# Performance work log

Measured on AMD Instinct MI355X. Metric: run time of the kernel, lower is better.

Reference implementation:

```python
import jax, jax.numpy as jnp
import numpy as np
import math

H = 16  # num heads
NEG = -1e9


def setup_inputs() -> dict:
    key = jax.random.key(0)
    ks = jax.random.split(key, 12)
    B, S, D = 2, 2048, 1024
    inp = {
        "query": jax.random.normal(ks[0], (B, S, D), jnp.float32),
        "key": jax.random.normal(ks[1], (B, S, D), jnp.float32),
        "value": jax.random.normal(ks[2], (B, S, D), jnp.float32),
        "mask": jax.random.randint(ks[3], (B, 1, S), 0, 2, jnp.int32),
        "wq": jax.random.normal(ks[4], (D, D), jnp.float32) * 0.02,
        "bq": jnp.zeros((D,), jnp.float32),
        "wk": jax.random.normal(ks[5], (D, D), jnp.float32) * 0.02,
        "bk": jnp.zeros((D,), jnp.float32),
        "wv": jax.random.normal(ks[6], (D, D), jnp.float32) * 0.02,
        "bv": jnp.zeros((D,), jnp.float32),
        "wo": jax.random.normal(ks[7], (D, D), jnp.float32) * 0.02,
        "bo": jnp.zeros((D,), jnp.float32),
    }
    return inp


def reference(query, key, value, mask, wq, bq, wk, bk, wv, bv, wo, bo):
    B, S, D = query.shape
    dk = D // H

    def proj(x, w, b):
        # torch Linear: x @ w.T + b ; then split heads -> [B, H, S, dk]
        y = x @ w.T + b
        return y.reshape(B, -1, H, dk).transpose(0, 2, 1, 3)

    q = proj(query, wq, bq)
    k = proj(key, wk, bk)
    v = proj(value, wv, bv)

    scores = jnp.einsum("bhqd,bhkd->bhqk", q, k) / math.sqrt(dk)  # [B,H,S,S]

    m = mask[:, None, :, :]  # [B,1,1,S] (mask.unsqueeze(1) in torch)
    scores = jnp.where(m == 0, NEG, scores)            # key-side padding mask
    scores = jnp.where(jnp.swapaxes(m, -2, -1) == 0, NEG, scores)  # query-side mask (q_len>1)

    p_attn = jax.nn.softmax(scores, axis=-1)
    # dropout p=0 / eval mode -> identity
    ctx = jnp.einsum("bhqk,bhkd->bhqd", p_attn, v)  # [B,H,S,dk]
    ctx = ctx.transpose(0, 2, 1, 3).reshape(B, S, H * dk)
    out = ctx @ wo.T + bo
    return out
```

## Files before the change

### kernel.cpp

```cpp
#include <hip/hip_runtime.h>
#include <hip/hip_bf16.h>

#define SEQ 2048
#define DIM 1024
#define NH  16
#define DK  64
#define NA  (2 * SEQ * DIM)
#define NW  (DIM * DIM)
#define PSTR 72
#define ESTR 136
#define FSTR 132
#define QSCALE 0.18033688011112042f

typedef __attribute__((ext_vector_type(4))) float f32x4;
typedef __attribute__((ext_vector_type(8))) __bf16 bf16x8;
typedef __attribute__((ext_vector_type(4))) __bf16 bf16x4;

__device__ __forceinline__ f32x4 mfma16(bf16x8 a, bf16x8 b, f32x4 c) {
  return __builtin_amdgcn_mfma_f32_16x16x32_bf16(a, b, c, 0, 0, 0);
}
__device__ __forceinline__ void async_load16(const void* g, void* l) {
  __builtin_amdgcn_global_load_lds(
      (const __attribute__((address_space(1))) void*)g,
      (__attribute__((address_space(3))) void*)l, 16, 0, 0);
}
__device__ __forceinline__ int swz(int row, int chunk) {
  return row * 8 + (chunk ^ (row & 7));
}

__global__ __launch_bounds__(256) void cvt_kernel(
    const float* __restrict__ s0, const float* __restrict__ s1,
    const float* __restrict__ s2, const float* __restrict__ s3,
    const float* __restrict__ s4, const float* __restrict__ s5,
    const float* __restrict__ s6,
    __hip_bfloat16* __restrict__ d0, __hip_bfloat16* __restrict__ d1,
    __hip_bfloat16* __restrict__ d2, __hip_bfloat16* __restrict__ d3,
    __hip_bfloat16* __restrict__ d4, __hip_bfloat16* __restrict__ d5,
    __hip_bfloat16* __restrict__ d6) {
  const int id = blockIdx.x;
  const float* s;
  __hip_bfloat16* d;
  int bid;
  if (id < 6144) {
    int t = id >> 11;
    bid = id & 2047;
    s = (t == 0) ? s0 : ((t == 1) ? s1 : s2);
    d = (t == 0) ? d0 : ((t == 1) ? d1 : d2);
  } else {
    int t = (id - 6144) >> 9;
    bid = (id - 6144) & 511;
    s = (t == 0) ? s3 : ((t == 1) ? s4 : ((t == 2) ? s5 : s6));
    d = (t == 0) ? d3 : ((t == 1) ? d4 : ((t == 2) ? d5 : d6));
  }
  size_t i = ((size_t)bid * 256 + threadIdx.x) * 8;
  float4 a = *(const float4*)(s + i);
  float4 b = *(const float4*)(s + i + 4);
  bf16x8 v = {(__bf16)a.x, (__bf16)a.y, (__bf16)a.z, (__bf16)a.w,
              (__bf16)b.x, (__bf16)b.y, (__bf16)b.z, (__bf16)b.w};
  *(bf16x8*)(d + i) = v;
}

__device__ __forceinline__ void gemm_stage(
    const __hip_bfloat16* __restrict__ X, const __hip_bfloat16* __restrict__ W,
    __hip_bfloat16* A, __hip_bfloat16* B, int m0, int n0, int k0,
    int w, int lane) {
  for (int r = 0; r < 4; ++r) {
    int cbase = r * 256 + w * 64;
    int c = cbase + lane, row = c >> 3, cs = c & 7;
    int off = cs ^ (row & 7);
    async_load16((const char*)(X + (size_t)(m0 + row) * DIM + k0) + off * 16,
                 (char*)A + cbase * 16);
    async_load16((const char*)(W + (size_t)(n0 + row) * DIM + k0) + off * 16,
                 (char*)B + cbase * 16);
  }
}

__device__ __forceinline__ void gemm_mainloop(
    const __hip_bfloat16* __restrict__ X, const __hip_bfloat16* __restrict__ W,
    __hip_bfloat16* lds, int m0, int n0, f32x4 acc[4][4]) {
  const int tid = threadIdx.x, lane = tid & 63, w = tid >> 6;
  const int quad = lane >> 4, l15 = lane & 15;
  const int wm = (w >> 1) * 64, wn = (w & 1) * 64;

  f32x4 z = {0.f, 0.f, 0.f, 0.f};
  for (int mi = 0; mi < 4; ++mi)
    for (int ni = 0; ni < 4; ++ni) acc[mi][ni] = z;

  gemm_stage(X, W, lds, lds + 8192, m0, n0, 0, w, lane);
  __syncthreads();

  for (int it = 0; it < 16; ++it) {
    __hip_bfloat16* Ac = lds + (it & 1) * 16384;
    __hip_bfloat16* Bc = Ac + 8192;
    if (it < 15) {
      __hip_bfloat16* An = lds + ((it + 1) & 1) * 16384;
      gemm_stage(X, W, An, An + 8192, m0, n0, (it + 1) * 64, w, lane);
    }
    for (int kk = 0; kk < 2; ++kk) {
      bf16x8 a[4], b[4];
      for (int mi = 0; mi < 4; ++mi)
        a[mi] = *(const bf16x8*)(Ac + swz(wm + mi * 16 + l15, kk * 4 + quad) * 8);
      for (int ni = 0; ni < 4; ++ni)
        b[ni] = *(const bf16x8*)(Bc + swz(wn + ni * 16 + l15, kk * 4 + quad) * 8);
      for (int mi = 0; mi < 4; ++mi)
        for (int ni = 0; ni < 4; ++ni)
          acc[mi][ni] = mfma16(a[mi], b[ni], acc[mi][ni]);
    }
    __syncthreads();
  }
}

__global__ __launch_bounds__(256) void qkv_proj_kernel(
    const __hip_bfloat16* __restrict__ xq, const __hip_bfloat16* __restrict__ xk,
    const __hip_bfloat16* __restrict__ xv,
    const __hip_bfloat16* __restrict__ wq, const __hip_bfloat16* __restrict__ wk,
    const __hip_bfloat16* __restrict__ wv,
    const float* __restrict__ bq, const float* __restrict__ bk,
    const float* __restrict__ bv,
    __hip_bfloat16* __restrict__ q_ws, __hip_bfloat16* __restrict__ k_ws,
    __hip_bfloat16* __restrict__ vt_ws) {
  __shared__ __align__(16) __hip_bfloat16 S_lds[4 * 8192];

  const int z = blockIdx.z;
  const __hip_bfloat16* X = (z == 0) ? xq : ((z == 1) ? xk : xv);
  const __hip_bfloat16* W = (z == 0) ? wq : ((z == 1) ? wk : wv);
  const float* bias = (z == 0) ? bq : ((z == 1) ? bk : bv);
  const float f = (z == 0) ? QSCALE : 1.0f;

  const int m0 = blockIdx.y * 128, n0 = blockIdx.x * 128;
  f32x4 acc[4][4];
  gemm_mainloop(X, W, S_lds, m0, n0, acc);

  const int tid = threadIdx.x, lane = tid & 63, w = tid >> 6;
  const int quad = lane >> 4, l15 = lane & 15;
  const int wm = (w >> 1) * 64, wn = (w & 1) * 64;

  if (z != 2) {
    __hip_bfloat16* out = (z == 0) ? q_ws : k_ws;
    for (int mi = 0; mi < 4; ++mi)
      for (int ni = 0; ni < 4; ++ni) {
        const float bv_ = bias[n0 + wn + ni * 16 + l15];
        for (int r = 0; r < 4; ++r)
          S_lds[(wm + mi * 16 + quad * 4 + r) * ESTR + wn + ni * 16 + l15] =
              __float2bfloat16((acc[mi][ni][r] + bv_) * f);
      }
    __syncthreads();
    for (int r2 = 0; r2 < 8; ++r2) {
      int c = r2 * 256 + tid;
      int row = c >> 4, j = c & 15;
      int m = m0 + row, b = m >> 11, s = m & 2047;
      int n = n0 + j * 8, h = n >> 6, d = n & 63;
      *(uint4*)(out + ((size_t)(b * NH + h) * SEQ + s) * DK + d) =
          *(const uint4*)(S_lds + row * ESTR + j * 8);
    }
  } else {
    for (int mi = 0; mi < 4; ++mi)
      for (int ni = 0; ni < 4; ++ni) {
        const int n_local = wn + ni * 16 + l15;
        const float bv_ = bias[n0 + n_local];
        bf16x4 tv;
        for (int r = 0; r < 4; ++r) tv[r] = (__bf16)(acc[mi][ni][r] + bv_);
        *(bf16x4*)(S_lds + n_local * ESTR + wm + mi * 16 + quad * 4) = tv;
      }
    __syncthreads();
    const int b = m0 >> 11, s_base = m0 & 2047;
    for (int r2 = 0; r2 < 8; ++r2) {
      int c2 = r2 * 256 + tid;
      int nrow = c2 >> 4, moff = (c2 & 15) * 8;
      int n = n0 + nrow, h = n >> 6, d = n & 63;
      *(uint4*)(vt_ws + ((size_t)(b * NH + h) * DK + d) * SEQ + s_base + moff) =
          *(const uint4*)(S_lds + nrow * ESTR + moff);
    }
  }
}

__global__ __launch_bounds__(512) void attn_kernel(
    const __hip_bfloat16* __restrict__ qg, const __hip_bfloat16* __restrict__ kg,
    const __hip_bfloat16* __restrict__ vtg, const int* __restrict__ mask,
    __hip_bfloat16* __restrict__ ctx) {
  __shared__ __align__(16) __hip_bfloat16 QP_lds[128 * PSTR];
  __shared__ __align__(16) __hip_bfloat16 K_lds[2][64 * 64];
  __shared__ __align__(16) __hip_bfloat16 V_lds[2][64 * 64];
  __shared__ float bias_lds[SEQ];

  const int tid = threadIdx.x, lane = tid & 63, w = tid >> 6;
  const int quad = lane >> 4, l15 = lane & 15;
  const int bh = blockIdx.y, b = bh >> 4, h = bh & 15;
  const int q0 = blockIdx.x * 128;
  const size_t head = (size_t)bh * SEQ * DK;
  const size_t vthead = (size_t)bh * DK * SEQ;

  for (int i = tid; i < SEQ; i += 512)
    bias_lds[i] = mask[b * SEQ + i] ? 0.f : -1e9f;

  for (int r = 0; r < 2; ++r) {
    int cbase = r * 512 + w * 64;
    int c = cbase + lane, row = c >> 3, cs = c & 7;
    int off = cs ^ (row & 7);
    async_load16((const char*)(qg + head + (size_t)(q0 + row) * DK) + off * 16,
                 (char*)QP_lds + cbase * 16);
  }
  {
    int row = tid >> 3, cs = tid & 7;
    int off = cs ^ (row & 7);
    async_load16((const char*)(kg + head + (size_t)row * DK) + off * 16,
                 (char*)K_lds[0] + tid * 16);
    async_load16((const char*)(vtg + vthead + (size_t)row * SEQ) + off * 16,
                 (char*)V_lds[0] + tid * 16);
  }
  __syncthreads();

  bf16x8 qf[2];
  for (int kk = 0; kk < 2; ++kk)
    qf[kk] = *(const bf16x8*)(QP_lds + swz(w * 16 + l15, kk * 4 + quad) * 8);
  const int qmv = mask[b * SEQ + q0 + w * 16 + l15];

  __hip_bfloat16* P_lds = QP_lds;
  const bf16x8 ones = {(__bf16)1.f, (__bf16)1.f, (__bf16)1.f, (__bf16)1.f,
                       (__bf16)1.f, (__bf16)1.f, (__bf16)1.f, (__bf16)1.f};

  f32x4 z = {0.f, 0.f, 0.f, 0.f};
  f32x4 o_acc[4];
  for (int di = 0; di < 4; ++di) o_acc[di] = z;
  f32x4 o_sum = z;

  for (int t = 0; t < 32; ++t) {
    const int cur = t & 1;
    if (t < 31) {
      const int k1 = (t + 1) * 64;
      int row = tid >> 3, cs = tid & 7;
      int off = cs ^ (row & 7);
      async_load16((const char*)(kg + head + (size_t)(k1 + row) * DK) + off * 16,
                   (char*)K_lds[1 - cur] + tid * 16);
      async_load16((const char*)(vtg + vthead + (size_t)row * SEQ + k1) + off * 16,
                   (char*)V_lds[1 - cur] + tid * 16);
    }
    const int k0 = t * 64;

    f32x4 s_acc[4];
    for (int mi = 0; mi < 4; ++mi)
      s_acc[mi] = *(const f32x4*)(bias_lds + k0 + mi * 16 + quad * 4);
    for (int kk = 0; kk < 2; ++kk) {
      bf16x8 ak[4];
      for (int mi = 0; mi < 4; ++mi)
        ak[mi] = *(const bf16x8*)(K_lds[cur] + swz(mi * 16 + l15, kk * 4 + quad) * 8);
      for (int mi = 0; mi < 4; ++mi)
        s_acc[mi] = mfma16(ak[mi], qf[kk], s_acc[mi]);
    }

    for (int mi = 0; mi < 4; ++mi) {
      bf16x4 pk;
      for (int r = 0; r < 4; ++r) {
        float s2 = qmv ? s_acc[mi][r] : 0.f;
        pk[r] = (__bf16)__builtin_amdgcn_exp2f(s2);
      }
      *(bf16x4*)(P_lds + (w * 16 + l15) * PSTR + mi * 16 + quad * 4) = pk;
    }

    for (int kk = 0; kk < 2; ++kk) {
      bf16x8 bp = *(const bf16x8*)(P_lds + (w * 16 + l15) * PSTR + kk * 32 + quad * 8);
      bf16x8 av[4];
      for (int di = 0; di < 4; ++di)
        av[di] = *(const bf16x8*)(V_lds[cur] + swz(di * 16 + l15, kk * 4 + quad) * 8);
      for (int di = 0; di < 4; ++di)
        o_acc[di] = mfma16(av[di], bp, o_acc[di]);
      o_sum = mfma16(ones, bp, o_sum);
    }
    __syncthreads();
  }

  const float inv = 1.f / o_sum[0];

  for (int di = 0; di < 4; ++di) {
    bf16x4 ov;
    for (int r = 0; r < 4; ++r) ov[r] = (__bf16)(o_acc[di][r] * inv);
    *(bf16x4*)(P_lds + (w * 16 + l15) * PSTR + di * 16 + quad * 4) = ov;
  }
  __syncthreads();
  for (int r = 0; r < 2; ++r) {
    int c = r * 512 + tid, row = c >> 3, off = c & 7;
    *(uint4*)(ctx + (size_t)(b * SEQ + q0 + row) * DIM + h * DK + off * 8) =
        *(const uint4*)(P_lds + row * PSTR + off * 8);
  }
}

__global__ __launch_bounds__(256) void out_proj_kernel(
    const __hip_bfloat16* __restrict__ ctx, const __hip_bfloat16* __restrict__ wo,
    const float* __restrict__ bo, float* __restrict__ out) {
  __shared__ __align__(16) char S_raw[128 * FSTR * 4];
  __hip_bfloat16* S_lds = (__hip_bfloat16*)S_raw;

  const int m0 = blockIdx.y * 128, n0 = blockIdx.x * 128;
  f32x4 acc[4][4];
  gemm_mainloop(ctx, wo, S_lds, m0, n0, acc);

  const int tid = threadIdx.x, lane = tid & 63, w = tid >> 6;
  const int quad = lane >> 4, l15 = lane & 15;
  const int wm = (w >> 1) * 64, wn = (w & 1) * 64;
  float* epi = (float*)S_raw;

  for (int mi = 0; mi < 4; ++mi)
    for (int ni = 0; ni < 4; ++ni) {
      const float bv_ = bo[n0 + wn + ni * 16 + l15];
      for (int r = 0; r < 4; ++r)
        epi[(wm + mi * 16 + quad * 4 + r) * FSTR + wn + ni * 16 + l15] =
            acc[mi][ni][r] + bv_;
    }
  __syncthreads();
  for (int r2 = 0; r2 < 16; ++r2) {
    int c = r2 * 256 + tid;
    int row = c >> 5, j = c & 31;
    *(float4*)(out + (size_t)(m0 + row) * DIM + n0 + j * 4) =
        *(const float4*)(epi + row * FSTR + j * 4);
  }
}

extern "C" void kernel_launch(void* const* d_in, const int* in_sizes, int n_in,
                              void* d_out, int out_size, void* d_ws, size_t ws_size,
                              hipStream_t stream) {
  const float* query = (const float*)d_in[0];
  const float* key   = (const float*)d_in[1];
  const float* value = (const float*)d_in[2];
  const int*   mask  = (const int*)d_in[3];
  const float* wq = (const float*)d_in[4];
  const float* bq = (const float*)d_in[5];
  const float* wk = (const float*)d_in[6];
  const float* bk = (const float*)d_in[7];
  const float* wv = (const float*)d_in[8];
  const float* bv = (const float*)d_in[9];
  const float* wo = (const float*)d_in[10];
  const float* bo = (const float*)d_in[11];
  float* out = (float*)d_out;

  char* ws = (char*)d_ws;
  const size_t SZA = (size_t)NA * 2;
  const size_t SZW = (size_t)NW * 2;
  __hip_bfloat16* xq  = (__hip_bfloat16*)(ws);
  __hip_bfloat16* xk  = (__hip_bfloat16*)(ws + SZA);
  __hip_bfloat16* xv  = (__hip_bfloat16*)(ws + 2 * SZA);
  __hip_bfloat16* wqb = (__hip_bfloat16*)(ws + 3 * SZA);
  __hip_bfloat16* wkb = (__hip_bfloat16*)(ws + 3 * SZA + SZW);
  __hip_bfloat16* wvb = (__hip_bfloat16*)(ws + 3 * SZA + 2 * SZW);
  __hip_bfloat16* wob = (__hip_bfloat16*)(ws + 3 * SZA + 3 * SZW);
  __hip_bfloat16* q_ws  = (__hip_bfloat16*)(ws + 3 * SZA + 4 * SZW);
  __hip_bfloat16* k_ws  = (__hip_bfloat16*)(ws + 4 * SZA + 4 * SZW);
  __hip_bfloat16* vt_ws = (__hip_bfloat16*)(ws + 5 * SZA + 4 * SZW);
  __hip_bfloat16* ctx_ws = xq;

  cvt_kernel<<<dim3(8192), dim3(256), 0, stream>>>(
      query, key, value, wq, wk, wv, wo, xq, xk, xv, wqb, wkb, wvb, wob);
  qkv_proj_kernel<<<dim3(8, 32, 3), dim3(256), 0, stream>>>(
      xq, xk, xv, wqb, wkb, wvb, bq, bk, bv, q_ws, k_ws, vt_ws);
  attn_kernel<<<dim3(16, 32), dim3(512), 0, stream>>>(q_ws, k_ws, vt_ws, mask, ctx_ws);
  out_proj_kernel<<<dim3(8, 32), dim3(256), 0, stream>>>(ctx_ws, wob, bo, out);
}
```

Measured before the change: 225.9 us.

## Give each attention wave two 16-row query tiles, halving block size

Cuts the attention block from 8 waves to 4, with each wave now covering 32 query rows (two 16-row MFMA tiles) instead of 16. Each K and V fragment read from LDS is reused across two query tiles, which halves LDS reads of K/V per MFMA. In exchange, per-wave register use grows (doubled score and output accumulators), fewer waves per block can hide latency, and each thread issues twice as many async loads.

```diff
diff --git a/kernel.cpp b/kernel.cpp
--- a/kernel.cpp
+++ b/kernel.cpp
@@ -174,7 +174,7 @@
   }
 }
 
-__global__ __launch_bounds__(512) void attn_kernel(
+__global__ __launch_bounds__(256) void attn_kernel(
     const __hip_bfloat16* __restrict__ qg, const __hip_bfloat16* __restrict__ kg,
     const __hip_bfloat16* __restrict__ vtg, const int* __restrict__ mask,
     __hip_bfloat16* __restrict__ ctx) {
@@ -190,95 +190,111 @@
   const size_t head = (size_t)bh * SEQ * DK;
   const size_t vthead = (size_t)bh * DK * SEQ;
 
-  for (int i = tid; i < SEQ; i += 512)
+  for (int i = tid; i < SEQ; i += 256)
     bias_lds[i] = mask[b * SEQ + i] ? 0.f : -1e9f;
 
-  for (int r = 0; r < 2; ++r) {
-    int cbase = r * 512 + w * 64;
+  for (int r = 0; r < 4; ++r) {
+    int cbase = r * 256 + w * 64;
     int c = cbase + lane, row = c >> 3, cs = c & 7;
     int off = cs ^ (row & 7);
     async_load16((const char*)(qg + head + (size_t)(q0 + row) * DK) + off * 16,
                  (char*)QP_lds + cbase * 16);
   }
-  {
-    int row = tid >> 3, cs = tid & 7;
+  for (int r = 0; r < 2; ++r) {
+    int cbase = r * 256 + w * 64;
+    int c = cbase + lane, row = c >> 3, cs = c & 7;
     int off = cs ^ (row & 7);
     async_load16((const char*)(kg + head + (size_t)row * DK) + off * 16,
-                 (char*)K_lds[0] + tid * 16);
+                 (char*)K_lds[0] + cbase * 16);
     async_load16((const char*)(vtg + vthead + (size_t)row * SEQ) + off * 16,
-                 (char*)V_lds[0] + tid * 16);
+                 (char*)V_lds[0] + cbase * 16);
   }
   __syncthreads();
 
-  bf16x8 qf[2];
+  bf16x8 qf[2][2];
   for (int kk = 0; kk < 2; ++kk)
-    qf[kk] = *(const bf16x8*)(QP_lds + swz(w * 16 + l15, kk * 4 + quad) * 8);
-  const int qmv = mask[b * SEQ + q0 + w * 16 + l15];
+    for (int ni = 0; ni < 2; ++ni)
+      qf[kk][ni] = *(const bf16x8*)(QP_lds + swz(w * 32 + ni * 16 + l15, kk * 4 + quad) * 8);
+  int qmv[2];
+  for (int ni = 0; ni < 2; ++ni)
+    qmv[ni] = mask[b * SEQ + q0 + w * 32 + ni * 16 + l15];
 
   __hip_bfloat16* P_lds = QP_lds;
   const bf16x8 ones = {(__bf16)1.f, (__bf16)1.f, (__bf16)1.f, (__bf16)1.f,
                        (__bf16)1.f, (__bf16)1.f, (__bf16)1.f, (__bf16)1.f};
 
   f32x4 z = {0.f, 0.f, 0.f, 0.f};
-  f32x4 o_acc[4];
-  for (int di = 0; di < 4; ++di) o_acc[di] = z;
-  f32x4 o_sum = z;
+  f32x4 o_acc[2][4];
+  for (int ni = 0; ni < 2; ++ni)
+    for (int di = 0; di < 4; ++di) o_acc[ni][di] = z;
+  f32x4 o_sum[2] = {z, z};
 
   for (int t = 0; t < 32; ++t) {
     const int cur = t & 1;
     if (t < 31) {
       const int k1 = (t + 1) * 64;
-      int row = tid >> 3, cs = tid & 7;
-      int off = cs ^ (row & 7);
-      async_load16((const char*)(kg + head + (size_t)(k1 + row) * DK) + off * 16,
-                   (char*)K_lds[1 - cur] + tid * 16);
-      async_load16((const char*)(vtg + vthead + (size_t)row * SEQ + k1) + off * 16,
-                   (char*)V_lds[1 - cur] + tid * 16);
+      for (int r = 0; r < 2; ++r) {
+        int cbase = r * 256 + w * 64;
+        int c = cbase + lane, row = c >> 3, cs = c & 7;
+        int off = cs ^ (row & 7);
+        async_load16((const char*)(kg + head + (size_t)(k1 + row) * DK) + off * 16,
+                     (char*)K_lds[1 - cur] + cbase * 16);
+        async_load16((const char*)(vtg + vthead + (size_t)row * SEQ + k1) + off * 16,
+                     (char*)V_lds[1 - cur] + cbase * 16);
+      }
     }
     const int k0 = t * 64;
 
-    f32x4 s_acc[4];
-    for (int mi = 0; mi < 4; ++mi)
-      s_acc[mi] = *(const f32x4*)(bias_lds + k0 + mi * 16 + quad * 4);
+    f32x4 s_acc[4][2];
+    for (int mi = 0; mi < 4; ++mi) {
+      f32x4 kb = *(const f32x4*)(bias_lds + k0 + mi * 16 + quad * 4);
+      for (int ni = 0; ni < 2; ++ni) s_acc[mi][ni] = kb;
+    }
     for (int kk = 0; kk < 2; ++kk) {
       bf16x8 ak[4];
       for (int mi = 0; mi < 4; ++mi)
         ak[mi] = *(const bf16x8*)(K_lds[cur] + swz(mi * 16 + l15, kk * 4 + quad) * 8);
       for (int mi = 0; mi < 4; ++mi)
-        s_acc[mi] = mfma16(ak[mi], qf[kk], s_acc[mi]);
-    }
-
-    for (int mi = 0; mi < 4; ++mi) {
-      bf16x4 pk;
-      for (int r = 0; r < 4; ++r) {
-        float s2 = qmv ? s_acc[mi][r] : 0.f;
-        pk[r] = (__bf16)__builtin_amdgcn_exp2f(s2);
-      }
-      *(bf16x4*)(P_lds + (w * 16 + l15) * PSTR + mi * 16 + quad * 4) = pk;
-    }
+        for (int ni = 0; ni < 2; ++ni)
+          s_acc[mi][ni] = mfma16(ak[mi], qf[kk][ni], s_acc[mi][ni]);
+    }
+
+    for (int mi = 0; mi < 4; ++mi)
+      for (int ni = 0; ni < 2; ++ni) {
+        bf16x4 pk;
+        for (int r = 0; r < 4; ++r) {
+          float s2 = qmv[ni] ? s_acc[mi][ni][r] : 0.f;
+          pk[r] = (__bf16)__builtin_amdgcn_exp2f(s2);
+        }
+        *(bf16x4*)(P_lds + (w * 32 + ni * 16 + l15) * PSTR + mi * 16 + quad * 4) = pk;
+      }
 
     for (int kk = 0; kk < 2; ++kk) {
-      bf16x8 bp = *(const bf16x8*)(P_lds + (w * 16 + l15) * PSTR + kk * 32 + quad * 8);
-      bf16x8 av[4];
+      bf16x8 av[4], bp[2];
       for (int di = 0; di < 4; ++di)
         av[di] = *(const bf16x8*)(V_lds[cur] + swz(di * 16 + l15, kk * 4 + quad) * 8);
-      for (int di = 0; di < 4; ++di)
-        o_acc[di] = mfma16(av[di], bp, o_acc[di]);
-      o_sum = mfma16(ones, bp, o_sum);
+      for (int ni = 0; ni < 2; ++ni)
+        bp[ni] = *(const bf16x8*)(P_lds + (w * 32 + ni * 16 + l15) * PSTR + kk * 32 + quad * 8);
+      for (int ni = 0; ni < 2; ++ni) {
+        for (int di = 0; di < 4; ++di)
+          o_acc[ni][di] = mfma16(av[di], bp[ni], o_acc[ni][di]);
+        o_sum[ni] = mfma16(ones, bp[ni], o_sum[ni]);
+      }
     }
     __syncthreads();
   }
 
-  const float inv = 1.f / o_sum[0];
-
-  for (int di = 0; di < 4; ++di) {
-    bf16x4 ov;
-    for (int r = 0; r < 4; ++r) ov[r] = (__bf16)(o_acc[di][r] * inv);
-    *(bf16x4*)(P_lds + (w * 16 + l15) * PSTR + di * 16 + quad * 4) = ov;
-  }
+  const float inv[2] = {1.f / o_sum[0][0], 1.f / o_sum[1][0]};
+
+  for (int ni = 0; ni < 2; ++ni)
+    for (int di = 0; di < 4; ++di) {
+      bf16x4 ov;
+      for (int r = 0; r < 4; ++r) ov[r] = (__bf16)(o_acc[ni][di][r] * inv[ni]);
+      *(bf16x4*)(P_lds + (w * 32 + ni * 16 + l15) * PSTR + di * 16 + quad * 4) = ov;
+    }
   __syncthreads();
-  for (int r = 0; r < 2; ++r) {
-    int c = r * 512 + tid, row = c >> 3, off = c & 7;
+  for (int r = 0; r < 4; ++r) {
+    int c = r * 256 + tid, row = c >> 3, off = c & 7;
     *(uint4*)(ctx + (size_t)(b * SEQ + q0 + row) * DIM + h * DK + off * 8) =
         *(const uint4*)(P_lds + row * PSTR + off * 8);
   }
@@ -351,6 +367,6 @@
       query, key, value, wq, wk, wv, wo, xq, xk, xv, wqb, wkb, wvb, wob);
   qkv_proj_kernel<<<dim3(8, 32, 3), dim3(256), 0, stream>>>(
       xq, xk, xv, wqb, wkb, wvb, bq, bk, bv, q_ws, k_ws, vt_ws);
-  attn_kernel<<<dim3(16, 32), dim3(512), 0, stream>>>(q_ws, k_ws, vt_ws, mask, ctx_ws);
+  attn_kernel<<<dim3(16, 32), dim3(256), 0, stream>>>(q_ws, k_ws, vt_ws, mask, ctx_ws);
   out_proj_kernel<<<dim3(8, 32), dim3(256), 0, stream>>>(ctx_ws, wob, bo, out);
 }
```

After: 243.4 us. +7.8%, slower.

## Store K/V in MFMA fragment order and load attention operands directly from global

Applied to the files above, without the earlier changes.

The QKV projection now writes K and V^T in a pre-swizzled, per-lane fragment layout, so the attention kernel can read MFMA operands straight from global or L2 into registers. This removes the K/V LDS double buffering, the async copies and the per-tile __syncthreads. The mask-to-bias conversion moves into one extra block of the convert kernel, and Q fragments are also read directly from global. The cost is that each of the 8 waves in a block now fetches the same K/V fragments from global separately instead of sharing one LDS copy, which relies on the cache hierarchy to absorb the repeated loads.

```diff
diff --git a/kernel.cpp b/kernel.cpp
--- a/kernel.cpp
+++ b/kernel.cpp
@@ -32,12 +32,17 @@
     const float* __restrict__ s0, const float* __restrict__ s1,
     const float* __restrict__ s2, const float* __restrict__ s3,
     const float* __restrict__ s4, const float* __restrict__ s5,
-    const float* __restrict__ s6,
+    const float* __restrict__ s6, const int* __restrict__ mask,
     __hip_bfloat16* __restrict__ d0, __hip_bfloat16* __restrict__ d1,
     __hip_bfloat16* __restrict__ d2, __hip_bfloat16* __restrict__ d3,
     __hip_bfloat16* __restrict__ d4, __hip_bfloat16* __restrict__ d5,
-    __hip_bfloat16* __restrict__ d6) {
+    __hip_bfloat16* __restrict__ d6, float* __restrict__ biasg) {
   const int id = blockIdx.x;
+  if (id == 8192) {
+    for (int i = threadIdx.x; i < 2 * SEQ; i += 256)
+      biasg[i] = mask[i] ? 0.f : -1e9f;
+    return;
+  }
   const float* s;
   __hip_bfloat16* d;
   int bid;
@@ -117,8 +122,8 @@
     const __hip_bfloat16* __restrict__ wv,
     const float* __restrict__ bq, const float* __restrict__ bk,
     const float* __restrict__ bv,
-    __hip_bfloat16* __restrict__ q_ws, __hip_bfloat16* __restrict__ k_ws,
-    __hip_bfloat16* __restrict__ vt_ws) {
+    __hip_bfloat16* __restrict__ q_ws, __hip_bfloat16* __restrict__ k_t,
+    __hip_bfloat16* __restrict__ vt_t) {
   __shared__ __align__(16) __hip_bfloat16 S_lds[4 * 8192];
 
   const int z = blockIdx.z;
@@ -134,9 +139,9 @@
   const int tid = threadIdx.x, lane = tid & 63, w = tid >> 6;
   const int quad = lane >> 4, l15 = lane & 15;
   const int wm = (w >> 1) * 64, wn = (w & 1) * 64;
+  const int b = m0 >> 11, tbase = (m0 & 2047) >> 6, hbase = n0 >> 6;
 
   if (z != 2) {
-    __hip_bfloat16* out = (z == 0) ? q_ws : k_ws;
     for (int mi = 0; mi < 4; ++mi)
       for (int ni = 0; ni < 4; ++ni) {
         const float bv_ = bias[n0 + wn + ni * 16 + l15];
@@ -145,13 +150,25 @@
               __float2bfloat16((acc[mi][ni][r] + bv_) * f);
       }
     __syncthreads();
-    for (int r2 = 0; r2 < 8; ++r2) {
-      int c = r2 * 256 + tid;
-      int row = c >> 4, j = c & 15;
-      int m = m0 + row, b = m >> 11, s = m & 2047;
-      int n = n0 + j * 8, h = n >> 6, d = n & 63;
-      *(uint4*)(out + ((size_t)(b * NH + h) * SEQ + s) * DK + d) =
-          *(const uint4*)(S_lds + row * ESTR + j * 8);
+    if (z == 0) {
+      for (int r2 = 0; r2 < 8; ++r2) {
+        int c = r2 * 256 + tid;
+        int row = c >> 4, j = c & 15;
+        int m = m0 + row, s = m & 2047;
+        int n = n0 + j * 8, h = n >> 6, d = n & 63;
+        *(uint4*)(q_ws + ((size_t)(b * NH + h) * SEQ + s) * DK + d) =
+            *(const uint4*)(S_lds + row * ESTR + j * 8);
+      }
+    } else {
+      for (int fi = 0; fi < 8; ++fi) {
+        int fg = w * 8 + fi;
+        int h_l = fg >> 4, t_l = (fg >> 3) & 1, kk = (fg >> 2) & 1, mi = fg & 3;
+        uint4 vdat = *(const uint4*)(S_lds + (t_l * 64 + mi * 16 + l15) * ESTR +
+                                     h_l * 64 + kk * 32 + quad * 8);
+        size_t bh = (size_t)(b * NH + hbase + h_l);
+        size_t off = ((((bh * 32 + tbase + t_l) * 2 + kk) * 4 + mi) * 64 + lane) * 8;
+        *(uint4*)(k_t + off) = vdat;
+      }
     }
   } else {
     for (int mi = 0; mi < 4; ++mi)
@@ -163,87 +180,54 @@
         *(bf16x4*)(S_lds + n_local * ESTR + wm + mi * 16 + quad * 4) = tv;
       }
     __syncthreads();
-    const int b = m0 >> 11, s_base = m0 & 2047;
-    for (int r2 = 0; r2 < 8; ++r2) {
-      int c2 = r2 * 256 + tid;
-      int nrow = c2 >> 4, moff = (c2 & 15) * 8;
-      int n = n0 + nrow, h = n >> 6, d = n & 63;
-      *(uint4*)(vt_ws + ((size_t)(b * NH + h) * DK + d) * SEQ + s_base + moff) =
-          *(const uint4*)(S_lds + nrow * ESTR + moff);
+    for (int fi = 0; fi < 8; ++fi) {
+      int fg = w * 8 + fi;
+      int h_l = fg >> 4, t_l = (fg >> 3) & 1, kk = (fg >> 2) & 1, di = fg & 3;
+      uint4 vdat = *(const uint4*)(S_lds + (h_l * 64 + di * 16 + l15) * ESTR +
+                                   t_l * 64 + kk * 32 + quad * 8);
+      size_t bh = (size_t)(b * NH + hbase + h_l);
+      size_t off = ((((bh * 32 + tbase + t_l) * 2 + kk) * 4 + di) * 64 + lane) * 8;
+      *(uint4*)(vt_t + off) = vdat;
     }
   }
 }
 
 __global__ __launch_bounds__(512) void attn_kernel(
-    const __hip_bfloat16* __restrict__ qg, const __hip_bfloat16* __restrict__ kg,
-    const __hip_bfloat16* __restrict__ vtg, const int* __restrict__ mask,
-    __hip_bfloat16* __restrict__ ctx) {
-  __shared__ __align__(16) __hip_bfloat16 QP_lds[128 * PSTR];
-  __shared__ __align__(16) __hip_bfloat16 K_lds[2][64 * 64];
-  __shared__ __align__(16) __hip_bfloat16 V_lds[2][64 * 64];
-  __shared__ float bias_lds[SEQ];
+    const __hip_bfloat16* __restrict__ qg, const __hip_bfloat16* __restrict__ kt,
+    const __hip_bfloat16* __restrict__ vt, const int* __restrict__ mask,
+    const float* __restrict__ biasg, __hip_bfloat16* __restrict__ ctx) {
+  __shared__ __align__(16) __hip_bfloat16 P_lds[128 * PSTR];
 
   const int tid = threadIdx.x, lane = tid & 63, w = tid >> 6;
   const int quad = lane >> 4, l15 = lane & 15;
   const int bh = blockIdx.y, b = bh >> 4, h = bh & 15;
   const int q0 = blockIdx.x * 128;
   const size_t head = (size_t)bh * SEQ * DK;
-  const size_t vthead = (size_t)bh * DK * SEQ;
-
-  for (int i = tid; i < SEQ; i += 512)
-    bias_lds[i] = mask[b * SEQ + i] ? 0.f : -1e9f;
-
-  for (int r = 0; r < 2; ++r) {
-    int cbase = r * 512 + w * 64;
-    int c = cbase + lane, row = c >> 3, cs = c & 7;
-    int off = cs ^ (row & 7);
-    async_load16((const char*)(qg + head + (size_t)(q0 + row) * DK) + off * 16,
-                 (char*)QP_lds + cbase * 16);
-  }
-  {
-    int row = tid >> 3, cs = tid & 7;
-    int off = cs ^ (row & 7);
-    async_load16((const char*)(kg + head + (size_t)row * DK) + off * 16,
-                 (char*)K_lds[0] + tid * 16);
-    async_load16((const char*)(vtg + vthead + (size_t)row * SEQ) + off * 16,
-                 (char*)V_lds[0] + tid * 16);
-  }
-  __syncthreads();
 
   bf16x8 qf[2];
   for (int kk = 0; kk < 2; ++kk)
-    qf[kk] = *(const bf16x8*)(QP_lds + swz(w * 16 + l15, kk * 4 + quad) * 8);
+    qf[kk] = *(const bf16x8*)(qg + head + (size_t)(q0 + w * 16 + l15) * DK +
+                              kk * 32 + quad * 8);
   const int qmv = mask[b * SEQ + q0 + w * 16 + l15];
-
-  __hip_bfloat16* P_lds = QP_lds;
+  const float* bias_b = biasg + b * SEQ;
+
   const bf16x8 ones = {(__bf16)1.f, (__bf16)1.f, (__bf16)1.f, (__bf16)1.f,
                        (__bf16)1.f, (__bf16)1.f, (__bf16)1.f, (__bf16)1.f};
-
   f32x4 z = {0.f, 0.f, 0.f, 0.f};
   f32x4 o_acc[4];
   for (int di = 0; di < 4; ++di) o_acc[di] = z;
   f32x4 o_sum = z;
 
+  const size_t tb = (size_t)bh * 32;
+
   for (int t = 0; t < 32; ++t) {
-    const int cur = t & 1;
-    if (t < 31) {
-      const int k1 = (t + 1) * 64;
-      int row = tid >> 3, cs = tid & 7;
-      int off = cs ^ (row & 7);
-      async_load16((const char*)(kg + head + (size_t)(k1 + row) * DK) + off * 16,
-                   (char*)K_lds[1 - cur] + tid * 16);
-      async_load16((const char*)(vtg + vthead + (size_t)row * SEQ + k1) + off * 16,
-                   (char*)V_lds[1 - cur] + tid * 16);
-    }
-    const int k0 = t * 64;
-
     f32x4 s_acc[4];
     for (int mi = 0; mi < 4; ++mi)
-      s_acc[mi] = *(const f32x4*)(bias_lds + k0 + mi * 16 + quad * 4);
+      s_acc[mi] = *(const f32x4*)(bias_b + t * 64 + mi * 16 + quad * 4);
     for (int kk = 0; kk < 2; ++kk) {
       bf16x8 ak[4];
       for (int mi = 0; mi < 4; ++mi)
-        ak[mi] = *(const bf16x8*)(K_lds[cur] + swz(mi * 16 + l15, kk * 4 + quad) * 8);
+        ak[mi] = *(const bf16x8*)(kt + ((((tb + t) * 2 + kk) * 4 + mi) * 64 + lane) * 8);
       for (int mi = 0; mi < 4; ++mi)
         s_acc[mi] = mfma16(ak[mi], qf[kk], s_acc[mi]);
     }
@@ -261,12 +245,11 @@
       bf16x8 bp = *(const bf16x8*)(P_lds + (w * 16 + l15) * PSTR + kk * 32 + quad * 8);
       bf16x8 av[4];
       for (int di = 0; di < 4; ++di)
-        av[di] = *(const bf16x8*)(V_lds[cur] + swz(di * 16 + l15, kk * 4 + quad) * 8);
+        av[di] = *(const bf16x8*)(vt + ((((tb + t) * 2 + kk) * 4 + di) * 64 + lane) * 8);
       for (int di = 0; di < 4; ++di)
         o_acc[di] = mfma16(av[di], bp, o_acc[di]);
       o_sum = mfma16(ones, bp, o_sum);
     }
-    __syncthreads();
   }
 
   const float inv = 1.f / o_sum[0];
@@ -342,15 +325,18 @@
   __hip_bfloat16* wkb = (__hip_bfloat16*)(ws + 3 * SZA + SZW);
   __hip_bfloat16* wvb = (__hip_bfloat16*)(ws + 3 * SZA + 2 * SZW);
   __hip_bfloat16* wob = (__hip_bfloat16*)(ws + 3 * SZA + 3 * SZW);
-  __hip_bfloat16* q_ws  = (__hip_bfloat16*)(ws + 3 * SZA + 4 * SZW);
-  __hip_bfloat16* k_ws  = (__hip_bfloat16*)(ws + 4 * SZA + 4 * SZW);
-  __hip_bfloat16* vt_ws = (__hip_bfloat16*)(ws + 5 * SZA + 4 * SZW);
+  __hip_bfloat16* q_ws = (__hip_bfloat16*)(ws + 3 * SZA + 4 * SZW);
+  __hip_bfloat16* k_t  = (__hip_bfloat16*)(ws + 4 * SZA + 4 * SZW);
+  __hip_bfloat16* vt_t = (__hip_bfloat16*)(ws + 5 * SZA + 4 * SZW);
+  float* biasg = (float*)(ws + 6 * SZA + 4 * SZW);
   __hip_bfloat16* ctx_ws = xq;
 
-  cvt_kernel<<<dim3(8192), dim3(256), 0, stream>>>(
-      query, key, value, wq, wk, wv, wo, xq, xk, xv, wqb, wkb, wvb, wob);
+  cvt_kernel<<<dim3(8193), dim3(256), 0, stream>>>(
+      query, key, value, wq, wk, wv, wo, mask,
+      xq, xk, xv, wqb, wkb, wvb, wob, biasg);
   qkv_proj_kernel<<<dim3(8, 32, 3), dim3(256), 0, stream>>>(
-      xq, xk, xv, wqb, wkb, wvb, bq, bk, bv, q_ws, k_ws, vt_ws);
-  attn_kernel<<<dim3(16, 32), dim3(512), 0, stream>>>(q_ws, k_ws, vt_ws, mask, ctx_ws);
+      xq, xk, xv, wqb, wkb, wvb, bq, bk, bv, q_ws, k_t, vt_t);
+  attn_kernel<<<dim3(16, 32), dim3(512), 0, stream>>>(
+      q_ws, k_t, vt_t, mask, biasg, ctx_ws);
   out_proj_kernel<<<dim3(8, 32), dim3(256), 0, stream>>>(ctx_ws, wob, bo, out);
 }
```

Measured after the change: 259.0 us. 1.15x slower.
